# Optimization experiments

Measured on AMD Instinct MI355X. Metric: run time of the kernel, lower is better.

## Reference

```python
import jax, jax.numpy as jnp
import numpy as np

B, T, C, F = 512, 1024, 8, 8
ISIZE = C * F  # 64
OSIZE = 64


def setup_inputs() -> dict:
    key = jax.random.key(0)
    k_x, k_w, k_b = jax.random.split(key, 3)
    x = jax.random.normal(k_x, (B, T, C, F), dtype=jnp.float32)
    # per-group Linear params, torch nn.Linear layout: weight [osize, isize], bias [osize]
    bound = 1.0 / np.sqrt(ISIZE)
    W = jax.random.uniform(k_w, (T, OSIZE, ISIZE), dtype=jnp.float32, minval=-bound, maxval=bound)
    b = jax.random.uniform(k_b, (T, OSIZE), dtype=jnp.float32, minval=-bound, maxval=bound)
    return {"x": x, "W": W, "b": b}


def reference(x, W, b):
    # collapseDims: cat(x.split(1, 2), 3).squeeze(2) == reshape [B,T,C,F] -> [B,T,C*F]
    Bn, Tn, Cn, Fn = x.shape
    xc = x.reshape(Bn, Tn, Cn * Fn)
    # per-slice Linear along dim=1 (T groups): y[b,t,:] = xc[b,t,:] @ W[t].T + b[t]
    out = jnp.einsum("bti,toi->bto", xc, W) + b[None, :, :]
    return out
```

## Files before the change

### kernel.cpp

```cpp
#include <hip/hip_runtime.h>


#define T_DIM 1024
#define B_DIM 512
#define KSZ 64
#define OSZ 64
#define ROWS 64
#define NCH (B_DIM / ROWS)

typedef __attribute__((ext_vector_type(8))) short short8;
typedef __attribute__((ext_vector_type(4))) float f32x4;

static __device__ __forceinline__ unsigned short f2bf(float f) {
    unsigned u = __float_as_uint(f);
    u += 0x7FFFu + ((u >> 16) & 1u);
    return (unsigned short)(u >> 16);
}
static __device__ __forceinline__ float bf2f(unsigned short h) {
    return __uint_as_float((unsigned)h << 16);
}

#define LGKM_BARRIER() do {                                   \
    asm volatile("s_waitcnt lgkmcnt(0)" ::: "memory");        \
    __builtin_amdgcn_s_barrier();                             \
} while (0)

__global__ __launch_bounds__(256, 4) void pl_kernel(
    const float* __restrict__ x,
    const float* __restrict__ W,
    const float* __restrict__ bias,
    float* __restrict__ out)
{
    __shared__ short Xh[ROWS * KSZ];
    __shared__ short Xl[ROWS * KSZ];
    __shared__ short Wh[OSZ * KSZ];
    __shared__ short Wl[OSZ * KSZ];

    const int t   = blockIdx.x;
    const int tid = threadIdx.x;

    const int sr = tid >> 2;
    const int kc = tid & 3;
    const int w  = tid >> 6;
    const int l  = tid & 63;
    const int n  = l & 15;
    const int kq = l >> 4;

    const size_t cstep = (size_t)ROWS * T_DIM * KSZ;
    const float* xp0 = x + ((size_t)sr * T_DIM + t) * KSZ + 16 * kc;

    float4 pf0 = *(const float4*)(xp0);
    float4 pf1 = *(const float4*)(xp0 + 4);
    float4 pf2 = *(const float4*)(xp0 + 8);
    float4 pf3 = *(const float4*)(xp0 + 12);

    {
        const float* wp = W + (size_t)t * (OSZ * KSZ) + (size_t)sr * KSZ + 16 * kc;
        float4 g0 = *(const float4*)(wp);
        float4 g1 = *(const float4*)(wp + 4);
        float4 g2 = *(const float4*)(wp + 8);
        float4 g3 = *(const float4*)(wp + 12);
        float a[8]  = {g0.x, g0.y, g0.z, g0.w, g1.x, g1.y, g1.z, g1.w};
        float b2[8] = {g2.x, g2.y, g2.z, g2.w, g3.x, g3.y, g3.z, g3.w};
        short8 h0, l0, h1, l1;
        #pragma unroll
        for (int j = 0; j < 8; ++j) {
            unsigned short hh = f2bf(a[j]);
            h0[j] = (short)hh; l0[j] = (short)f2bf(a[j] - bf2f(hh));
            unsigned short h2 = f2bf(b2[j]);
            h1[j] = (short)h2; l1[j] = (short)f2bf(b2[j] - bf2f(h2));
        }
        const int p0 = (((2 * kc)     ^ (sr & 7)) << 3);
        const int p1 = (((2 * kc + 1) ^ (sr & 7)) << 3);
        *(short8*)&Wh[sr * KSZ + p0] = h0;
        *(short8*)&Wl[sr * KSZ + p0] = l0;
        *(short8*)&Wh[sr * KSZ + p1] = h1;
        *(short8*)&Wl[sr * KSZ + p1] = l1;
    }

    float bv[4];
    #pragma unroll
    for (int ct = 0; ct < 4; ++ct)
        bv[ct] = bias[(size_t)t * OSZ + 16 * ct + n];

    const int p0 = (((2 * kc)     ^ (sr & 7)) << 3);
    const int p1 = (((2 * kc + 1) ^ (sr & 7)) << 3);

    for (int c = 0; c < NCH; ++c) {
        float a[8]  = {pf0.x, pf0.y, pf0.z, pf0.w, pf1.x, pf1.y, pf1.z, pf1.w};
        float b2[8] = {pf2.x, pf2.y, pf2.z, pf2.w, pf3.x, pf3.y, pf3.z, pf3.w};
        short8 h0, l0, h1, l1;
        #pragma unroll
        for (int j = 0; j < 8; ++j) {
            unsigned short hh = f2bf(a[j]);
            h0[j] = (short)hh; l0[j] = (short)f2bf(a[j] - bf2f(hh));
            unsigned short h2 = f2bf(b2[j]);
            h1[j] = (short)h2; l1[j] = (short)f2bf(b2[j] - bf2f(h2));
        }

        if (c > 0) LGKM_BARRIER();

        *(short8*)&Xh[sr * KSZ + p0] = h0;
        *(short8*)&Xl[sr * KSZ + p0] = l0;
        *(short8*)&Xh[sr * KSZ + p1] = h1;
        *(short8*)&Xl[sr * KSZ + p1] = l1;

        if (c + 1 < NCH) {
            const float* xp = xp0 + (size_t)(c + 1) * cstep;
            pf0 = *(const float4*)(xp);
            pf1 = *(const float4*)(xp + 4);
            pf2 = *(const float4*)(xp + 8);
            pf3 = *(const float4*)(xp + 12);
        }

        LGKM_BARRIER();

        const int arow = 16 * w + n;
        short8 ah[2], al[2];
        #pragma unroll
        for (int ks = 0; ks < 2; ++ks) {
            const int pos = ((ks * 4 + kq) ^ (arow & 7)) << 3;
            ah[ks] = *(const short8*)&Xh[arow * KSZ + pos];
            al[ks] = *(const short8*)&Xl[arow * KSZ + pos];
        }

        f32x4 acc[4] = {};
        #pragma unroll
        for (int ct = 0; ct < 4; ++ct) {
            const int brow = 16 * ct + n;
            #pragma unroll
            for (int ks = 0; ks < 2; ++ks) {
                const int pos = ((ks * 4 + kq) ^ (brow & 7)) << 3;
                short8 bh = *(const short8*)&Wh[brow * KSZ + pos];
                short8 bl = *(const short8*)&Wl[brow * KSZ + pos];
                acc[ct] = __builtin_amdgcn_mfma_f32_16x16x32_bf16(ah[ks], bh, acc[ct], 0, 0, 0);
                acc[ct] = __builtin_amdgcn_mfma_f32_16x16x32_bf16(al[ks], bh, acc[ct], 0, 0, 0);
                acc[ct] = __builtin_amdgcn_mfma_f32_16x16x32_bf16(ah[ks], bl, acc[ct], 0, 0, 0);
            }
        }

        const int row0 = c * ROWS;
        #pragma unroll
        for (int ct = 0; ct < 4; ++ct) {
            #pragma unroll
            for (int j = 0; j < 4; ++j) {
                const size_t b = (size_t)row0 + 16 * w + 4 * kq + j;
                out[(b * T_DIM + t) * OSZ + 16 * ct + n] = acc[ct][j] + bv[ct];
            }
        }
    }
}

extern "C" void kernel_launch(void* const* d_in, const int* in_sizes, int n_in,
                              void* d_out, int out_size, void* d_ws, size_t ws_size,
                              hipStream_t stream) {
    const float* x    = (const float*)d_in[0];
    const float* W    = (const float*)d_in[1];
    const float* bias = (const float*)d_in[2];
    float* out        = (float*)d_out;

    dim3 grid(T_DIM);
    dim3 block(256);
    pl_kernel<<<grid, block, 0, stream>>>(x, W, bias, out);
}
```

Before: 64.42 us.

## Double-buffer X tiles in LDS and hoist W fragments into registers

```diff
diff --git a/kernel.cpp b/kernel.cpp
--- a/kernel.cpp
+++ b/kernel.cpp
@@ -25,14 +25,14 @@
     __builtin_amdgcn_s_barrier();                             \
 } while (0)
 
-__global__ __launch_bounds__(256, 4) void pl_kernel(
+__global__ __launch_bounds__(256, 3) void pl_kernel(
     const float* __restrict__ x,
     const float* __restrict__ W,
     const float* __restrict__ bias,
     float* __restrict__ out)
 {
-    __shared__ short Xh[ROWS * KSZ];
-    __shared__ short Xl[ROWS * KSZ];
+    __shared__ short Xh[2][ROWS * KSZ];
+    __shared__ short Xl[2][ROWS * KSZ];
     __shared__ short Wh[OSZ * KSZ];
     __shared__ short Wl[OSZ * KSZ];
 
@@ -54,6 +54,9 @@
     float4 pf2 = *(const float4*)(xp0 + 8);
     float4 pf3 = *(const float4*)(xp0 + 12);
 
+    const int p0 = (((2 * kc)     ^ (sr & 7)) << 3);
+    const int p1 = (((2 * kc + 1) ^ (sr & 7)) << 3);
+
     {
         const float* wp = W + (size_t)t * (OSZ * KSZ) + (size_t)sr * KSZ + 16 * kc;
         float4 g0 = *(const float4*)(wp);
@@ -70,12 +73,24 @@
             unsigned short h2 = f2bf(b2[j]);
             h1[j] = (short)h2; l1[j] = (short)f2bf(b2[j] - bf2f(h2));
         }
-        const int p0 = (((2 * kc)     ^ (sr & 7)) << 3);
-        const int p1 = (((2 * kc + 1) ^ (sr & 7)) << 3);
         *(short8*)&Wh[sr * KSZ + p0] = h0;
         *(short8*)&Wl[sr * KSZ + p0] = l0;
         *(short8*)&Wh[sr * KSZ + p1] = h1;
         *(short8*)&Wl[sr * KSZ + p1] = l1;
+    }
+
+    LGKM_BARRIER();
+
+    short8 wfh[4][2], wfl[4][2];
+    #pragma unroll
+    for (int ct = 0; ct < 4; ++ct) {
+        const int brow = 16 * ct + n;
+        #pragma unroll
+        for (int ks = 0; ks < 2; ++ks) {
+            const int pos = ((ks * 4 + kq) ^ (brow & 7)) << 3;
+            wfh[ct][ks] = *(const short8*)&Wh[brow * KSZ + pos];
+            wfl[ct][ks] = *(const short8*)&Wl[brow * KSZ + pos];
+        }
     }
 
     float bv[4];
@@ -83,27 +98,27 @@
     for (int ct = 0; ct < 4; ++ct)
         bv[ct] = bias[(size_t)t * OSZ + 16 * ct + n];
 
-    const int p0 = (((2 * kc)     ^ (sr & 7)) << 3);
-    const int p1 = (((2 * kc + 1) ^ (sr & 7)) << 3);
+    #pragma unroll 2
+    for (int c = 0; c < NCH; ++c) {
+        short* xh = &Xh[c & 1][0];
+        short* xl = &Xl[c & 1][0];
 
-    for (int c = 0; c < NCH; ++c) {
-        float a[8]  = {pf0.x, pf0.y, pf0.z, pf0.w, pf1.x, pf1.y, pf1.z, pf1.w};
-        float b2[8] = {pf2.x, pf2.y, pf2.z, pf2.w, pf3.x, pf3.y, pf3.z, pf3.w};
-        short8 h0, l0, h1, l1;
-        #pragma unroll
-        for (int j = 0; j < 8; ++j) {
-            unsigned short hh = f2bf(a[j]);
-            h0[j] = (short)hh; l0[j] = (short)f2bf(a[j] - bf2f(hh));
-            unsigned short h2 = f2bf(b2[j]);
-            h1[j] = (short)h2; l1[j] = (short)f2bf(b2[j] - bf2f(h2));
+        {
+            float a[8]  = {pf0.x, pf0.y, pf0.z, pf0.w, pf1.x, pf1.y, pf1.z, pf1.w};
+            float b2[8] = {pf2.x, pf2.y, pf2.z, pf2.w, pf3.x, pf3.y, pf3.z, pf3.w};
+            short8 h0, l0, h1, l1;
+            #pragma unroll
+            for (int j = 0; j < 8; ++j) {
+                unsigned short hh = f2bf(a[j]);
+                h0[j] = (short)hh; l0[j] = (short)f2bf(a[j] - bf2f(hh));
+                unsigned short h2 = f2bf(b2[j]);
+                h1[j] = (short)h2; l1[j] = (short)f2bf(b2[j] - bf2f(h2));
+            }
+            *(short8*)&xh[sr * KSZ + p0] = h0;
+            *(short8*)&xl[sr * KSZ + p0] = l0;
+            *(short8*)&xh[sr * KSZ + p1] = h1;
+            *(short8*)&xl[sr * KSZ + p1] = l1;
         }
-
-        if (c > 0) LGKM_BARRIER();
-
-        *(short8*)&Xh[sr * KSZ + p0] = h0;
-        *(short8*)&Xl[sr * KSZ + p0] = l0;
-        *(short8*)&Xh[sr * KSZ + p1] = h1;
-        *(short8*)&Xl[sr * KSZ + p1] = l1;
 
         if (c + 1 < NCH) {
             const float* xp = xp0 + (size_t)(c + 1) * cstep;
@@ -120,22 +135,18 @@
         #pragma unroll
         for (int ks = 0; ks < 2; ++ks) {
             const int pos = ((ks * 4 + kq) ^ (arow & 7)) << 3;
-            ah[ks] = *(const short8*)&Xh[arow * KSZ + pos];
-            al[ks] = *(const short8*)&Xl[arow * KSZ + pos];
+            ah[ks] = *(const short8*)&xh[arow * KSZ + pos];
+            al[ks] = *(const short8*)&xl[arow * KSZ + pos];
         }
 
         f32x4 acc[4] = {};
         #pragma unroll
         for (int ct = 0; ct < 4; ++ct) {
-            const int brow = 16 * ct + n;
             #pragma unroll
             for (int ks = 0; ks < 2; ++ks) {
-                const int pos = ((ks * 4 + kq) ^ (brow & 7)) << 3;
-                short8 bh = *(const short8*)&Wh[brow * KSZ + pos];
-                short8 bl = *(const short8*)&Wl[brow * KSZ + pos];
-                acc[ct] = __builtin_amdgcn_mfma_f32_16x16x32_bf16(ah[ks], bh, acc[ct], 0, 0, 0);
-                acc[ct] = __builtin_amdgcn_mfma_f32_16x16x32_bf16(al[ks], bh, acc[ct], 0, 0, 0);
-                acc[ct] = __builtin_amdgcn_mfma_f32_16x16x32_bf16(ah[ks], bl, acc[ct], 0, 0, 0);
+                acc[ct] = __builtin_amdgcn_mfma_f32_16x16x32_bf16(ah[ks], wfh[ct][ks], acc[ct], 0, 0, 0);
+                acc[ct] = __builtin_amdgcn_mfma_f32_16x16x32_bf16(al[ks], wfh[ct][ks], acc[ct], 0, 0, 0);
+                acc[ct] = __builtin_amdgcn_mfma_f32_16x16x32_bf16(ah[ks], wfl[ct][ks], acc[ct], 0, 0, 0);
             }
         }
 
```

Measured after the change: 65.82 us. 2.2% more time.

## Load X directly into MFMA A-fragment registers, dropping LDS staging and barriers

Applied to the files above, without the earlier changes.

```diff
diff --git a/kernel.cpp b/kernel.cpp
--- a/kernel.cpp
+++ b/kernel.cpp
@@ -31,8 +31,6 @@
     const float* __restrict__ bias,
     float* __restrict__ out)
 {
-    __shared__ short Xh[ROWS * KSZ];
-    __shared__ short Xl[ROWS * KSZ];
     __shared__ short Wh[OSZ * KSZ];
     __shared__ short Wl[OSZ * KSZ];
 
@@ -46,20 +44,20 @@
     const int n  = l & 15;
     const int kq = l >> 4;
 
+    const float* wp = W + (size_t)t * (OSZ * KSZ) + (size_t)sr * KSZ + 16 * kc;
+    float4 g0 = *(const float4*)(wp);
+    float4 g1 = *(const float4*)(wp + 4);
+    float4 g2 = *(const float4*)(wp + 8);
+    float4 g3 = *(const float4*)(wp + 12);
+
+    const float* xA = x + ((size_t)(16 * w + n) * T_DIM + t) * KSZ + kq * 8;
     const size_t cstep = (size_t)ROWS * T_DIM * KSZ;
-    const float* xp0 = x + ((size_t)sr * T_DIM + t) * KSZ + 16 * kc;
-
-    float4 pf0 = *(const float4*)(xp0);
-    float4 pf1 = *(const float4*)(xp0 + 4);
-    float4 pf2 = *(const float4*)(xp0 + 8);
-    float4 pf3 = *(const float4*)(xp0 + 12);
+    float4 pa0 = *(const float4*)(xA);
+    float4 pa1 = *(const float4*)(xA + 4);
+    float4 pa2 = *(const float4*)(xA + 32);
+    float4 pa3 = *(const float4*)(xA + 36);
 
     {
-        const float* wp = W + (size_t)t * (OSZ * KSZ) + (size_t)sr * KSZ + 16 * kc;
-        float4 g0 = *(const float4*)(wp);
-        float4 g1 = *(const float4*)(wp + 4);
-        float4 g2 = *(const float4*)(wp + 8);
-        float4 g3 = *(const float4*)(wp + 12);
         float a[8]  = {g0.x, g0.y, g0.z, g0.w, g1.x, g1.y, g1.z, g1.w};
         float b2[8] = {g2.x, g2.y, g2.z, g2.w, g3.x, g3.y, g3.z, g3.w};
         short8 h0, l0, h1, l1;
@@ -78,64 +76,54 @@
         *(short8*)&Wl[sr * KSZ + p1] = l1;
     }
 
+    LGKM_BARRIER();
+
     float bv[4];
     #pragma unroll
     for (int ct = 0; ct < 4; ++ct)
         bv[ct] = bias[(size_t)t * OSZ + 16 * ct + n];
 
-    const int p0 = (((2 * kc)     ^ (sr & 7)) << 3);
-    const int p1 = (((2 * kc + 1) ^ (sr & 7)) << 3);
+    #pragma unroll 2
+    for (int c = 0; c < NCH; ++c) {
+        float4 na0, na1, na2, na3;
+        if (c + 1 < NCH) {
+            const float* xn = xA + (size_t)(c + 1) * cstep;
+            na0 = *(const float4*)(xn);
+            na1 = *(const float4*)(xn + 4);
+            na2 = *(const float4*)(xn + 32);
+            na3 = *(const float4*)(xn + 36);
+        }
 
-    for (int c = 0; c < NCH; ++c) {
-        float a[8]  = {pf0.x, pf0.y, pf0.z, pf0.w, pf1.x, pf1.y, pf1.z, pf1.w};
-        float b2[8] = {pf2.x, pf2.y, pf2.z, pf2.w, pf3.x, pf3.y, pf3.z, pf3.w};
-        short8 h0, l0, h1, l1;
+        float a[16] = {pa0.x, pa0.y, pa0.z, pa0.w, pa1.x, pa1.y, pa1.z, pa1.w,
+                       pa2.x, pa2.y, pa2.z, pa2.w, pa3.x, pa3.y, pa3.z, pa3.w};
+        short8 ah0, al0, ah1, al1;
         #pragma unroll
         for (int j = 0; j < 8; ++j) {
             unsigned short hh = f2bf(a[j]);
-            h0[j] = (short)hh; l0[j] = (short)f2bf(a[j] - bf2f(hh));
-            unsigned short h2 = f2bf(b2[j]);
-            h1[j] = (short)h2; l1[j] = (short)f2bf(b2[j] - bf2f(h2));
-        }
-
-        if (c > 0) LGKM_BARRIER();
-
-        *(short8*)&Xh[sr * KSZ + p0] = h0;
-        *(short8*)&Xl[sr * KSZ + p0] = l0;
-        *(short8*)&Xh[sr * KSZ + p1] = h1;
-        *(short8*)&Xl[sr * KSZ + p1] = l1;
-
-        if (c + 1 < NCH) {
-            const float* xp = xp0 + (size_t)(c + 1) * cstep;
-            pf0 = *(const float4*)(xp);
-            pf1 = *(const float4*)(xp + 4);
-            pf2 = *(const float4*)(xp + 8);
-            pf3 = *(const float4*)(xp + 12);
-        }
-
-        LGKM_BARRIER();
-
-        const int arow = 16 * w + n;
-        short8 ah[2], al[2];
-        #pragma unroll
-        for (int ks = 0; ks < 2; ++ks) {
-            const int pos = ((ks * 4 + kq) ^ (arow & 7)) << 3;
-            ah[ks] = *(const short8*)&Xh[arow * KSZ + pos];
-            al[ks] = *(const short8*)&Xl[arow * KSZ + pos];
+            ah0[j] = (short)hh; al0[j] = (short)f2bf(a[j] - bf2f(hh));
+            unsigned short h2 = f2bf(a[8 + j]);
+            ah1[j] = (short)h2; al1[j] = (short)f2bf(a[8 + j] - bf2f(h2));
         }
 
         f32x4 acc[4] = {};
         #pragma unroll
         for (int ct = 0; ct < 4; ++ct) {
             const int brow = 16 * ct + n;
-            #pragma unroll
-            for (int ks = 0; ks < 2; ++ks) {
-                const int pos = ((ks * 4 + kq) ^ (brow & 7)) << 3;
+            {
+                const int pos = (kq ^ (brow & 7)) << 3;
                 short8 bh = *(const short8*)&Wh[brow * KSZ + pos];
                 short8 bl = *(const short8*)&Wl[brow * KSZ + pos];
-                acc[ct] = __builtin_amdgcn_mfma_f32_16x16x32_bf16(ah[ks], bh, acc[ct], 0, 0, 0);
-                acc[ct] = __builtin_amdgcn_mfma_f32_16x16x32_bf16(al[ks], bh, acc[ct], 0, 0, 0);
-                acc[ct] = __builtin_amdgcn_mfma_f32_16x16x32_bf16(ah[ks], bl, acc[ct], 0, 0, 0);
+                acc[ct] = __builtin_amdgcn_mfma_f32_16x16x32_bf16(ah0, bh, acc[ct], 0, 0, 0);
+                acc[ct] = __builtin_amdgcn_mfma_f32_16x16x32_bf16(al0, bh, acc[ct], 0, 0, 0);
+                acc[ct] = __builtin_amdgcn_mfma_f32_16x16x32_bf16(ah0, bl, acc[ct], 0, 0, 0);
+            }
+            {
+                const int pos = ((4 + kq) ^ (brow & 7)) << 3;
+                short8 bh = *(const short8*)&Wh[brow * KSZ + pos];
+                short8 bl = *(const short8*)&Wl[brow * KSZ + pos];
+                acc[ct] = __builtin_amdgcn_mfma_f32_16x16x32_bf16(ah1, bh, acc[ct], 0, 0, 0);
+                acc[ct] = __builtin_amdgcn_mfma_f32_16x16x32_bf16(al1, bh, acc[ct], 0, 0, 0);
+                acc[ct] = __builtin_amdgcn_mfma_f32_16x16x32_bf16(ah1, bl, acc[ct], 0, 0, 0);
             }
         }
 
@@ -148,6 +136,8 @@
                 out[(b * T_DIM + t) * OSZ + 16 * ct + n] = acc[ct][j] + bv[ct];
             }
         }
+
+        if (c + 1 < NCH) { pa0 = na0; pa1 = na1; pa2 = na2; pa3 = na3; }
     }
 }
 
```

Measured after the change: 85.15 us. 32.2% more time.
